# Kernel optimization log

Hardware: AMD Instinct MI355X
Metric: run time of the kernel (lower is better)

The kernel has to match this reference:

```python
import jax, jax.numpy as jnp
import numpy as np

B, S, K, D = 512, 64, 8, 16
NE, NR, NU = 2_000_000, 64, 10_000
NSTEPS, NUNITS, NITER = 100, 128, 2


def _alpha_schedule():
    # betas = sigmoid(linspace(-6,6)) * (0.005 - 1e-5) + 1e-5; alphas_prod = cumprod(1-betas)
    betas = jax.nn.sigmoid(jnp.linspace(-6.0, 6.0, NSTEPS)) * (0.005 - 1e-5) + 1e-5
    aprod = jnp.cumprod(1.0 - betas)
    return jnp.sqrt(aprod), jnp.sqrt(1.0 - aprod)


def _forward(usr_emb, ent_emb, rel_emb, agg_W, agg_b, fc1_W, fc1_b, fc2_W, fc2_b,
             mlp_W1, mlp_b1, mlp_W2, mlp_b2, mlp_W3, mlp_b3, mlp_W4, mlp_b4,
             step_emb1, step_emb2, step_emb3, noise_e, u, v, click_seq, adj_ent, adj_rel, t):
    user = usr_emb[u]                                   # [B,D]
    # --- diffusion branch: x = x0*sqrt(abar_t) + e*sqrt(1-abar_t), then MLP with step-emb adds
    abar_sqrt, ombar_sqrt = _alpha_schedule()
    x = user * abar_sqrt[t][:, None] + noise_e * ombar_sqrt[t][:, None]
    for Wl, bl, se in ((mlp_W1, mlp_b1, step_emb1), (mlp_W2, mlp_b2, step_emb2), (mlp_W3, mlp_b3, step_emb3)):
        x = jax.nn.relu(x @ Wl + bl + se[t])            # [B,128]
    diff_out = x @ mlp_W4 + mlp_b4                      # [B,D]
    # --- multi-hop neighbor gather (entities/relations per hop)
    e0 = click_seq                                      # [B,S]
    e1 = adj_ent[e0]                                    # [B,S,K]
    e2 = adj_ent[e1].reshape(B, S, K * K)               # [B,S,K*K]
    r0 = adj_rel[e0]                                    # [B,S,K]
    r1 = adj_rel[e1].reshape(B, S, K * K)               # [B,S,K*K]
    ev = [ent_emb[e0][:, :, None, :], ent_emb[e1], ent_emb[e2]]  # [B,S,1,D],[B,S,K,D],[B,S,K*K,D]
    rv = [rel_emb[r0], rel_emb[r1]]

    def aggregate(self_v, neigh_v, rel_v, act):
        # KGCN sum-aggregator: user-relation score softmax over neighbors, weighted sum, linear, act
        scores = jnp.mean(user[:, None, None, None, :] * rel_v, axis=-1)   # [B,S,n,K]
        p = jax.nn.softmax(scores, axis=-1)
        neigh_agg = jnp.einsum('bsnk,bsnkd->bsnd', p, neigh_v)             # [B,S,n,D]
        return act((self_v + neigh_agg) @ agg_W + agg_b)

    for i in range(NITER):
        act = jnp.tanh if i == NITER - 1 else jax.nn.sigmoid
        nxt = []
        for hop in range(NITER - i):
            n_self = ev[hop].shape[2]
            nv = ev[hop + 1].reshape(B, S, n_self, K, D)
            relv = rv[hop].reshape(B, S, n_self, K, D)
            nxt.append(aggregate(ev[hop], nv, relv, act))
        ev = nxt
    item_emb = jax.nn.relu(ev[0].reshape(B, S, D))      # relu applied twice in source == once
    trans = item_emb                                    # Transform treated as identity (code unavailable)
    s_sum = jax.nn.relu(jnp.sum(trans, axis=1))         # [B,D]
    s_max = jax.nn.relu(jnp.max(trans, axis=1))         # [B,D]
    fusion = jnp.concatenate([s_sum, s_max], axis=1)    # [B,2D]
    feat = jax.nn.relu(jax.nn.relu(fusion @ fc1_W + fc1_b) @ fc2_W + fc2_b)  # [B,D]
    outs = jax.nn.sigmoid(jnp.sum(feat * ent_emb[v], axis=1))               # [B]
    return jnp.concatenate([outs[:, None], diff_out], axis=1)               # [B,1+D]


def setup_inputs() -> dict:
    key = jax.random.key(0)
    ks = iter(jax.random.split(key, 32))
    nrm = lambda shape, s: jax.random.normal(next(ks), shape, dtype=jnp.float32) * s
    zf = lambda shape: jnp.zeros(shape, dtype=jnp.float32)
    ri = lambda shape, hi: jax.random.randint(next(ks), shape, 0, hi, dtype=jnp.int32)
    return {
        'usr_emb': nrm((NU, D), 0.1), 'ent_emb': nrm((NE, D), 0.1), 'rel_emb': nrm((NR, D), 0.1),
        'agg_W': nrm((D, D), 0.25), 'agg_b': zf((D,)),
        'fc1_W': nrm((2 * D, 64), 0.18), 'fc1_b': zf((64,)),
        'fc2_W': nrm((64, D), 0.125), 'fc2_b': zf((D,)),
        'mlp_W1': nrm((D, NUNITS), 0.25), 'mlp_b1': zf((NUNITS,)),
        'mlp_W2': nrm((NUNITS, NUNITS), 0.09), 'mlp_b2': zf((NUNITS,)),
        'mlp_W3': nrm((NUNITS, NUNITS), 0.09), 'mlp_b3': zf((NUNITS,)),
        'mlp_W4': nrm((NUNITS, D), 0.09), 'mlp_b4': zf((D,)),
        'step_emb1': nrm((NSTEPS, NUNITS), 0.1), 'step_emb2': nrm((NSTEPS, NUNITS), 0.1),
        'step_emb3': nrm((NSTEPS, NUNITS), 0.1),
        'noise_e': jax.random.normal(next(ks), (B, D), dtype=jnp.float32),
        'u': ri((B,), NU), 'v': ri((B,), NE), 'click_seq': ri((B, S), NE),
        'adj_ent': ri((NE, K), NE), 'adj_rel': ri((NE, K), NR), 't': ri((B,), NSTEPS),
    }


def reference(usr_emb, ent_emb, rel_emb, agg_W, agg_b, fc1_W, fc1_b, fc2_W, fc2_b,
              mlp_W1, mlp_b1, mlp_W2, mlp_b2, mlp_W3, mlp_b3, mlp_W4, mlp_b4,
              step_emb1, step_emb2, step_emb3, noise_e, u, v, click_seq, adj_ent, adj_rel, t):
    return _forward(usr_emb, ent_emb, rel_emb, agg_W, agg_b, fc1_W, fc1_b, fc2_W, fc2_b,
                    mlp_W1, mlp_b1, mlp_W2, mlp_b2, mlp_W3, mlp_b3, mlp_W4, mlp_b4,
                    step_emb1, step_emb2, step_emb3, noise_e, u, v, click_seq, adj_ent, adj_rel, t)
```

## Files before the change

### kernel.cpp

```cpp
#include <hip/hip_runtime.h>
#include <math.h>

namespace {
constexpr int B = 512, S = 64, K = 8, D = 16, NR = 64, NSTEPS = 100, NUNITS = 128;
}

#define WAVE_LDS_FENCE() __asm__ volatile("s_waitcnt lgkmcnt(0)" ::: "memory")

__global__ __launch_bounds__(256) void k_prep_all(
    const float* __restrict__ usr_emb, const float* __restrict__ rel_emb,
    const int* __restrict__ u, const int* __restrict__ click_seq,
    const int* __restrict__ adj_ent, const int* __restrict__ adj_rel,
    float* __restrict__ w_tab, int* __restrict__ e1s, int* __restrict__ r0s,
    float* __restrict__ sa, float* __restrict__ so)
{
    int b = blockIdx.x, t = threadIdx.x;
    if (t < 64) {
        const float* ur = usr_emb + (long)u[b] * D;
        const float* rr = rel_emb + t * D;
        float s = 0.f;
#pragma unroll
        for (int d = 0; d < D; ++d) s += ur[d] * rr[d];
        w_tab[b * NR + t] = s * (1.0f / 16.0f);
    } else if (t < 128) {
        int p = b * S + (t - 64);
        int e0 = click_seq[p];
        const int4* ae = (const int4*)(adj_ent + (long)e0 * K);
        const int4* ar = (const int4*)(adj_rel + (long)e0 * K);
        int4 a0 = ae[0], a1 = ae[1], b0 = ar[0], b1 = ar[1];
        int4* oe = (int4*)(e1s + (long)p * K);
        int4* orr = (int4*)(r0s + (long)p * K);
        oe[0] = a0; oe[1] = a1;
        orr[0] = b0; orr[1] = b1;
    } else if (b == 0 && (t - 128) < NSTEPS) {
        int i = t - 128;
        float prod = 1.0f;
        for (int jj = 0; jj <= i; ++jj) {
            float x = -6.0f + (float)jj * (12.0f / 99.0f);
            float sig = 1.0f / (1.0f + expf(-x));
            prod *= (1.0f - (sig * (0.005f - 1e-5f) + 1e-5f));
        }
        sa[i] = sqrtf(prod);
        so[i] = sqrtf(1.0f - prod);
    }
}

__global__ __launch_bounds__(256) void k_kgcn(
    const float* __restrict__ ent_emb,
    const float* __restrict__ w_tab,
    const int* __restrict__ click_seq,
    const int* __restrict__ adj_ent,
    const int* __restrict__ adj_rel,
    const int* __restrict__ e1s,
    const int* __restrict__ r0s,
    const float* __restrict__ agg_W,
    const float* __restrict__ agg_b,
    float* __restrict__ item)
{
    __shared__ float wb[4][NR];
    __shared__ float Ws[4][D][D + 1];
    __shared__ float bs[4][D];
    __shared__ float Ms[4][K][D + 1];
    __shared__ float h1s[4][K][D + 1];
    __shared__ float h0s[4][D];
    __shared__ float A0s[4][D];
    __shared__ float M1s[4][D];
    __shared__ float p0s[4][K];

    const int tid = threadIdx.x;
    const int w = tid >> 6;
    const int lane = tid & 63;
    const int p = blockIdx.x * 4 + w;
    const int b = p >> 6;
    const int k = lane >> 3, j = lane & 7;

    const int e0 = click_seq[p];
    const int e1k = e1s[(long)p * K + k];
    const int r0k = r0s[(long)p * K + k];
    const int e2kj = adj_ent[(long)e1k * K + j];
    const int r1kj = adj_rel[(long)e1k * K + j];

    {
        const float4 wv = ((const float4*)agg_W)[lane];
        int row = lane >> 2, col = (lane & 3) * 4;
        Ws[w][row][col] = wv.x; Ws[w][row][col + 1] = wv.y;
        Ws[w][row][col + 2] = wv.z; Ws[w][row][col + 3] = wv.w;
        wb[w][lane] = w_tab[b * NR + lane];
        if (lane < D) bs[w][lane] = agg_b[lane];
    }
    WAVE_LDS_FENCE();

    float s1 = wb[w][r1kj];
    float m1 = s1;
    m1 = fmaxf(m1, __shfl_xor(m1, 1));
    m1 = fmaxf(m1, __shfl_xor(m1, 2));
    m1 = fmaxf(m1, __shfl_xor(m1, 4));
    float ex = expf(s1 - m1);
    float den = ex;
    den += __shfl_xor(den, 1);
    den += __shfl_xor(den, 2);
    den += __shfl_xor(den, 4);
    float p1 = ex / den;

    float q2r[D], q1r[D], q0r[D];
    {
        const float4* q2p = (const float4*)(ent_emb + (long)e2kj * D);
        float4 a0 = q2p[0], a1 = q2p[1], a2 = q2p[2], a3 = q2p[3];
        q2r[0]=a0.x; q2r[1]=a0.y; q2r[2]=a0.z; q2r[3]=a0.w;
        q2r[4]=a1.x; q2r[5]=a1.y; q2r[6]=a1.z; q2r[7]=a1.w;
        q2r[8]=a2.x; q2r[9]=a2.y; q2r[10]=a2.z; q2r[11]=a2.w;
        q2r[12]=a3.x; q2r[13]=a3.y; q2r[14]=a3.z; q2r[15]=a3.w;
    }
    {
        const float4* q1p = (const float4*)(ent_emb + (long)e1k * D);
        float4 a0 = q1p[0], a1 = q1p[1], a2 = q1p[2], a3 = q1p[3];
        q1r[0]=a0.x; q1r[1]=a0.y; q1r[2]=a0.z; q1r[3]=a0.w;
        q1r[4]=a1.x; q1r[5]=a1.y; q1r[6]=a1.z; q1r[7]=a1.w;
        q1r[8]=a2.x; q1r[9]=a2.y; q1r[10]=a2.z; q1r[11]=a2.w;
        q1r[12]=a3.x; q1r[13]=a3.y; q1r[14]=a3.z; q1r[15]=a3.w;
    }
    {
        const float4* q0p = (const float4*)(ent_emb + (long)e0 * D);
        float4 a0 = q0p[0], a1 = q0p[1], a2 = q0p[2], a3 = q0p[3];
        q0r[0]=a0.x; q0r[1]=a0.y; q0r[2]=a0.z; q0r[3]=a0.w;
        q0r[4]=a1.x; q0r[5]=a1.y; q0r[6]=a1.z; q0r[7]=a1.w;
        q0r[8]=a2.x; q0r[9]=a2.y; q0r[10]=a2.z; q0r[11]=a2.w;
        q0r[12]=a3.x; q0r[13]=a3.y; q0r[14]=a3.z; q0r[15]=a3.w;
    }

    {
        float cur[16];
#pragma unroll
        for (int d = 0; d < 16; ++d) cur[d] = p1 * q2r[d];
        const bool b0 = (lane & 1), b1 = (lane & 2), b2 = (lane & 4);
        float n8[8];
#pragma unroll
        for (int d = 0; d < 8; ++d) {
            float snd = b0 ? cur[d] : cur[d + 8];
            float kp  = b0 ? cur[d + 8] : cur[d];
            n8[d] = kp + __shfl_xor(snd, 1);
        }
        float n4[4];
#pragma unroll
        for (int d = 0; d < 4; ++d) {
            float snd = b1 ? n8[d] : n8[d + 4];
            float kp  = b1 ? n8[d + 4] : n8[d];
            n4[d] = kp + __shfl_xor(snd, 2);
        }
        float a0 = (b2 ? n4[2] : n4[0]) + __shfl_xor(b2 ? n4[0] : n4[2], 4);
        float a1 = (b2 ? n4[3] : n4[1]) + __shfl_xor(b2 ? n4[1] : n4[3], 4);
        const int dbase = (b0 ? 8 : 0) + (b1 ? 4 : 0) + (b2 ? 2 : 0);
        Ms[w][k][dbase]     = q1r[dbase]     + a0;
        Ms[w][k][dbase + 1] = q1r[dbase + 1] + a1;
    }

    float s0 = wb[w][r0k];
    float m0 = s0;
    m0 = fmaxf(m0, __shfl_xor(m0, 8));
    m0 = fmaxf(m0, __shfl_xor(m0, 16));
    m0 = fmaxf(m0, __shfl_xor(m0, 32));
    float e0x = expf(s0 - m0);
    float d0 = e0x;
    d0 += __shfl_xor(d0, 8);
    d0 += __shfl_xor(d0, 16);
    d0 += __shfl_xor(d0, 32);
    float p0 = e0x / d0;
    if (j == 0) p0s[w][k] = p0;

    {
        float cur[16];
#pragma unroll
        for (int d = 0; d < 16; ++d) cur[d] = p0 * q1r[d];
        const bool c0 = (lane & 8), c1 = (lane & 16), c2 = (lane & 32);
        float n8[8];
#pragma unroll
        for (int d = 0; d < 8; ++d) {
            float snd = c0 ? cur[d] : cur[d + 8];
            float kp  = c0 ? cur[d + 8] : cur[d];
            n8[d] = kp + __shfl_xor(snd, 8);
        }
        float n4[4];
#pragma unroll
        for (int d = 0; d < 4; ++d) {
            float snd = c1 ? n8[d] : n8[d + 4];
            float kp  = c1 ? n8[d + 4] : n8[d];
            n4[d] = kp + __shfl_xor(snd, 16);
        }
        float a0 = (c2 ? n4[2] : n4[0]) + __shfl_xor(c2 ? n4[0] : n4[2], 32);
        float a1 = (c2 ? n4[3] : n4[1]) + __shfl_xor(c2 ? n4[1] : n4[3], 32);
        const int dbase = (c0 ? 8 : 0) + (c1 ? 4 : 0) + (c2 ? 2 : 0);
        if (j == 0) { A0s[w][dbase] = a0; A0s[w][dbase + 1] = a1; }
    }
    WAVE_LDS_FENCE();

#pragma unroll
    for (int o = lane; o < 128; o += 64) {
        int ko = o >> 4, dd = o & 15;
        float acc = bs[w][dd];
#pragma unroll
        for (int din = 0; din < D; ++din) acc += Ms[w][ko][din] * Ws[w][din][dd];
        h1s[w][ko][dd] = 1.0f / (1.0f + expf(-acc));
    }

    const int ddl = lane & 15;
    {
        float acc = bs[w][ddl];
#pragma unroll
        for (int din = 0; din < D; ++din)
            acc += (q0r[din] + A0s[w][din]) * Ws[w][din][ddl];
        if (lane < D) h0s[w][lane] = 1.0f / (1.0f + expf(-acc));
    }
    WAVE_LDS_FENCE();

    if (lane < D) {
        float m = h0s[w][lane];
#pragma unroll
        for (int kk = 0; kk < K; ++kk) m += p0s[w][kk] * h1s[w][kk][lane];
        M1s[w][lane] = m;
    }
    WAVE_LDS_FENCE();

    {
        float acc = bs[w][ddl];
#pragma unroll
        for (int din = 0; din < D; ++din) acc += M1s[w][din] * Ws[w][din][ddl];
        if (lane < D) item[(long)p * D + lane] = fmaxf(tanhf(acc), 0.0f);
    }
}

__global__ __launch_bounds__(128) void k_tail(
    const float* __restrict__ item,
    const float* __restrict__ fc1_W, const float* __restrict__ fc1_b,
    const float* __restrict__ fc2_W, const float* __restrict__ fc2_b,
    const float* __restrict__ ent_emb, const int* __restrict__ v,
    const float* __restrict__ usr_emb, const float* __restrict__ noise_e,
    const int* __restrict__ u, const int* __restrict__ t_arr,
    const float* __restrict__ W1, const float* __restrict__ b1,
    const float* __restrict__ W2, const float* __restrict__ b2,
    const float* __restrict__ W3, const float* __restrict__ b3,
    const float* __restrict__ W4, const float* __restrict__ b4,
    const float* __restrict__ se1, const float* __restrict__ se2,
    const float* __restrict__ se3,
    const float* __restrict__ sa, const float* __restrict__ so,
    float* __restrict__ out)
{
    __shared__ float x0[D];
    __shared__ float ha[NUNITS];
    __shared__ float hb[NUNITS];
    __shared__ float sm[S][D + 1];
    __shared__ float fus[2 * D];
    __shared__ float hid[64];
    __shared__ float feat_s[D];

    int b = blockIdx.x, t = threadIdx.x;
    int ts = t_arr[b];

    if (t < D)
        x0[t] = usr_emb[(long)u[b] * D + t] * sa[ts] + noise_e[(long)b * D + t] * so[ts];
    __syncthreads();

    float a = b1[t] + se1[(long)ts * NUNITS + t];
#pragma unroll
    for (int i = 0; i < D; ++i) a += x0[i] * W1[i * NUNITS + t];
    ha[t] = fmaxf(a, 0.0f);
    __syncthreads();

    a = b2[t] + se2[(long)ts * NUNITS + t];
    for (int i = 0; i < NUNITS; ++i) a += ha[i] * W2[i * NUNITS + t];
    hb[t] = fmaxf(a, 0.0f);
    __syncthreads();

    a = b3[t] + se3[(long)ts * NUNITS + t];
    for (int i = 0; i < NUNITS; ++i) a += hb[i] * W3[i * NUNITS + t];
    __syncthreads();
    ha[t] = fmaxf(a, 0.0f);
    __syncthreads();

    if (t < D) {
        float acc = b4[t];
        for (int i = 0; i < NUNITS; ++i) acc += ha[i] * W4[i * D + t];
        out[(long)b * 17 + 1 + t] = acc;
    }

    if (t < 64) {
        const float4* ip = (const float4*)(item + ((long)b * S + t) * D);
        float4 r0 = ip[0], r1 = ip[1], r2 = ip[2], r3 = ip[3];
        sm[t][0]=r0.x;  sm[t][1]=r0.y;  sm[t][2]=r0.z;  sm[t][3]=r0.w;
        sm[t][4]=r1.x;  sm[t][5]=r1.y;  sm[t][6]=r1.z;  sm[t][7]=r1.w;
        sm[t][8]=r2.x;  sm[t][9]=r2.y;  sm[t][10]=r2.z; sm[t][11]=r2.w;
        sm[t][12]=r3.x; sm[t][13]=r3.y; sm[t][14]=r3.z; sm[t][15]=r3.w;
    }
    __syncthreads();

    if (t < D) {
        float sv = 0.0f, mv = -1e30f;
        for (int ss = 0; ss < S; ++ss) {
            float x = sm[ss][t];
            sv += x;
            mv = fmaxf(mv, x);
        }
        fus[t] = fmaxf(sv, 0.0f);
        fus[D + t] = fmaxf(mv, 0.0f);
    }
    __syncthreads();

    if (t < 64) {
        float acc = fc1_b[t];
#pragma unroll
        for (int i = 0; i < 2 * D; ++i) acc += fus[i] * fc1_W[i * 64 + t];
        hid[t] = fmaxf(acc, 0.0f);
    }
    __syncthreads();

    if (t < D) {
        float f = fc2_b[t];
#pragma unroll
        for (int i = 0; i < 64; ++i) f += hid[i] * fc2_W[i * D + t];
        feat_s[t] = fmaxf(f, 0.0f);
    }
    __syncthreads();

    if (t < D) {
        float g = feat_s[t] * ent_emb[(long)v[b] * D + t];
        g += __shfl_xor(g, 1);
        g += __shfl_xor(g, 2);
        g += __shfl_xor(g, 4);
        g += __shfl_xor(g, 8);
        if (t == 0) out[(long)b * 17] = 1.0f / (1.0f + expf(-g));
    }
}

extern "C" void kernel_launch(void* const* d_in, const int* in_sizes, int n_in,
                              void* d_out, int out_size, void* d_ws, size_t ws_size,
                              hipStream_t stream) {
    const float* usr_emb = (const float*)d_in[0];
    const float* ent_emb = (const float*)d_in[1];
    const float* rel_emb = (const float*)d_in[2];
    const float* agg_W   = (const float*)d_in[3];
    const float* agg_b   = (const float*)d_in[4];
    const float* fc1_W   = (const float*)d_in[5];
    const float* fc1_b   = (const float*)d_in[6];
    const float* fc2_W   = (const float*)d_in[7];
    const float* fc2_b   = (const float*)d_in[8];
    const float* mlp_W1  = (const float*)d_in[9];
    const float* mlp_b1  = (const float*)d_in[10];
    const float* mlp_W2  = (const float*)d_in[11];
    const float* mlp_b2  = (const float*)d_in[12];
    const float* mlp_W3  = (const float*)d_in[13];
    const float* mlp_b3  = (const float*)d_in[14];
    const float* mlp_W4  = (const float*)d_in[15];
    const float* mlp_b4  = (const float*)d_in[16];
    const float* se1     = (const float*)d_in[17];
    const float* se2     = (const float*)d_in[18];
    const float* se3     = (const float*)d_in[19];
    const float* noise_e = (const float*)d_in[20];
    const int* u         = (const int*)d_in[21];
    const int* v         = (const int*)d_in[22];
    const int* click_seq = (const int*)d_in[23];
    const int* adj_ent   = (const int*)d_in[24];
    const int* adj_rel   = (const int*)d_in[25];
    const int* t         = (const int*)d_in[26];
    float* out = (float*)d_out;

    float* ws = (float*)d_ws;
    float* w_tab = ws;
    float* sa    = w_tab + B * NR;
    float* so    = sa + 128;
    float* item  = so + 128;
    int*   e1s   = (int*)(item + B * S * D);
    int*   r0s   = e1s + B * S * K;

    k_prep_all<<<B, 256, 0, stream>>>(usr_emb, rel_emb, u, click_seq, adj_ent, adj_rel,
                                      w_tab, e1s, r0s, sa, so);
    k_kgcn<<<(B * S) / 4, 256, 0, stream>>>(ent_emb, w_tab, click_seq, adj_ent, adj_rel,
                                            e1s, r0s, agg_W, agg_b, item);
    k_tail<<<B, 128, 0, stream>>>(item, fc1_W, fc1_b, fc2_W, fc2_b, ent_emb, v,
                                  usr_emb, noise_e, u, t, mlp_W1, mlp_b1, mlp_W2, mlp_b2,
                                  mlp_W3, mlp_b3, mlp_W4, mlp_b4, se1, se2, se3, sa, so, out);
}
```

Baseline: 337.4 us.

## Streamline KGCN aggregation LDS use and split tail MLP across 256 threads

The KGCN kernel now stores a transposed weight tile that each lane loads as a float4 column, and reads the relation-score row straight from global memory instead of staging it in LDS. Hop-1 outputs are combined with p0 through shuffles rather than LDS round trips, which removes two LDS fences and several shared arrays. The tail kernel doubles its block to 256 threads, splits the 128-wide matvecs into two halves reduced through shared memory, and runs the feature-pooling/fc branch alongside the diffusion MLP. This cuts per-block serial latency, at the cost of extra syncthreads and more register pressure from holding the weight column.

```diff
diff --git a/kernel.cpp b/kernel.cpp
--- a/kernel.cpp
+++ b/kernel.cpp
@@ -6,6 +6,16 @@
 }
 
 #define WAVE_LDS_FENCE() __asm__ volatile("s_waitcnt lgkmcnt(0)" ::: "memory")
+
+#define LOAD16(dst, ptr)                                                     \
+    {                                                                        \
+        const float4* _p = (const float4*)(ptr);                             \
+        float4 _a = _p[0], _b = _p[1], _c = _p[2], _d = _p[3];               \
+        dst[0] = _a.x;  dst[1] = _a.y;  dst[2] = _a.z;  dst[3] = _a.w;       \
+        dst[4] = _b.x;  dst[5] = _b.y;  dst[6] = _b.z;  dst[7] = _b.w;       \
+        dst[8] = _c.x;  dst[9] = _c.y;  dst[10] = _c.z; dst[11] = _c.w;      \
+        dst[12] = _d.x; dst[13] = _d.y; dst[14] = _d.z; dst[15] = _d.w;      \
+    }
 
 __global__ __launch_bounds__(256) void k_prep_all(
     const float* __restrict__ usr_emb, const float* __restrict__ rel_emb,
@@ -57,15 +67,11 @@
     const float* __restrict__ agg_b,
     float* __restrict__ item)
 {
-    __shared__ float wb[4][NR];
-    __shared__ float Ws[4][D][D + 1];
+    __shared__ __attribute__((aligned(16))) float Wt[4][D][20];
+    __shared__ __attribute__((aligned(16))) float Ms[4][K][20];
+    __shared__ __attribute__((aligned(16))) float A0s[4][D];
+    __shared__ __attribute__((aligned(16))) float M1s[4][D];
     __shared__ float bs[4][D];
-    __shared__ float Ms[4][K][D + 1];
-    __shared__ float h1s[4][K][D + 1];
-    __shared__ float h0s[4][D];
-    __shared__ float A0s[4][D];
-    __shared__ float M1s[4][D];
-    __shared__ float p0s[4][K];
 
     const int tid = threadIdx.x;
     const int w = tid >> 6;
@@ -83,50 +89,32 @@
     {
         const float4 wv = ((const float4*)agg_W)[lane];
         int row = lane >> 2, col = (lane & 3) * 4;
-        Ws[w][row][col] = wv.x; Ws[w][row][col + 1] = wv.y;
-        Ws[w][row][col + 2] = wv.z; Ws[w][row][col + 3] = wv.w;
-        wb[w][lane] = w_tab[b * NR + lane];
+        Wt[w][col][row]     = wv.x;
+        Wt[w][col + 1][row] = wv.y;
+        Wt[w][col + 2][row] = wv.z;
+        Wt[w][col + 3][row] = wv.w;
         if (lane < D) bs[w][lane] = agg_b[lane];
     }
-    WAVE_LDS_FENCE();
-
-    float s1 = wb[w][r1kj];
-    float m1 = s1;
-    m1 = fmaxf(m1, __shfl_xor(m1, 1));
-    m1 = fmaxf(m1, __shfl_xor(m1, 2));
-    m1 = fmaxf(m1, __shfl_xor(m1, 4));
-    float ex = expf(s1 - m1);
+
+    const float* wrow = w_tab + (long)b * NR;
+    const float s1 = wrow[r1kj];
+    const float s0 = wrow[r0k];
+
+    float m1x = s1;
+    m1x = fmaxf(m1x, __shfl_xor(m1x, 1));
+    m1x = fmaxf(m1x, __shfl_xor(m1x, 2));
+    m1x = fmaxf(m1x, __shfl_xor(m1x, 4));
+    float ex = expf(s1 - m1x);
     float den = ex;
     den += __shfl_xor(den, 1);
     den += __shfl_xor(den, 2);
     den += __shfl_xor(den, 4);
     float p1 = ex / den;
 
-    float q2r[D], q1r[D], q0r[D];
-    {
-        const float4* q2p = (const float4*)(ent_emb + (long)e2kj * D);
-        float4 a0 = q2p[0], a1 = q2p[1], a2 = q2p[2], a3 = q2p[3];
-        q2r[0]=a0.x; q2r[1]=a0.y; q2r[2]=a0.z; q2r[3]=a0.w;
-        q2r[4]=a1.x; q2r[5]=a1.y; q2r[6]=a1.z; q2r[7]=a1.w;
-        q2r[8]=a2.x; q2r[9]=a2.y; q2r[10]=a2.z; q2r[11]=a2.w;
-        q2r[12]=a3.x; q2r[13]=a3.y; q2r[14]=a3.z; q2r[15]=a3.w;
-    }
-    {
-        const float4* q1p = (const float4*)(ent_emb + (long)e1k * D);
-        float4 a0 = q1p[0], a1 = q1p[1], a2 = q1p[2], a3 = q1p[3];
-        q1r[0]=a0.x; q1r[1]=a0.y; q1r[2]=a0.z; q1r[3]=a0.w;
-        q1r[4]=a1.x; q1r[5]=a1.y; q1r[6]=a1.z; q1r[7]=a1.w;
-        q1r[8]=a2.x; q1r[9]=a2.y; q1r[10]=a2.z; q1r[11]=a2.w;
-        q1r[12]=a3.x; q1r[13]=a3.y; q1r[14]=a3.z; q1r[15]=a3.w;
-    }
-    {
-        const float4* q0p = (const float4*)(ent_emb + (long)e0 * D);
-        float4 a0 = q0p[0], a1 = q0p[1], a2 = q0p[2], a3 = q0p[3];
-        q0r[0]=a0.x; q0r[1]=a0.y; q0r[2]=a0.z; q0r[3]=a0.w;
-        q0r[4]=a1.x; q0r[5]=a1.y; q0r[6]=a1.z; q0r[7]=a1.w;
-        q0r[8]=a2.x; q0r[9]=a2.y; q0r[10]=a2.z; q0r[11]=a2.w;
-        q0r[12]=a3.x; q0r[13]=a3.y; q0r[14]=a3.z; q0r[15]=a3.w;
-    }
+    float q2r[16], q1r[16], q0r[16];
+    LOAD16(q2r, ent_emb + (long)e2kj * D);
+    LOAD16(q1r, ent_emb + (long)e1k * D);
+    LOAD16(q0r, ent_emb + (long)e0 * D);
 
     {
         float cur[16];
@@ -150,11 +138,9 @@
         float a0 = (b2 ? n4[2] : n4[0]) + __shfl_xor(b2 ? n4[0] : n4[2], 4);
         float a1 = (b2 ? n4[3] : n4[1]) + __shfl_xor(b2 ? n4[1] : n4[3], 4);
         const int dbase = (b0 ? 8 : 0) + (b1 ? 4 : 0) + (b2 ? 2 : 0);
-        Ms[w][k][dbase]     = q1r[dbase]     + a0;
-        Ms[w][k][dbase + 1] = q1r[dbase + 1] + a1;
-    }
-
-    float s0 = wb[w][r0k];
+        *(float2*)&Ms[w][k][dbase] = make_float2(q1r[dbase] + a0, q1r[dbase + 1] + a1);
+    }
+
     float m0 = s0;
     m0 = fmaxf(m0, __shfl_xor(m0, 8));
     m0 = fmaxf(m0, __shfl_xor(m0, 16));
@@ -165,7 +151,6 @@
     d0 += __shfl_xor(d0, 16);
     d0 += __shfl_xor(d0, 32);
     float p0 = e0x / d0;
-    if (j == 0) p0s[w][k] = p0;
 
     {
         float cur[16];
@@ -189,46 +174,65 @@
         float a0 = (c2 ? n4[2] : n4[0]) + __shfl_xor(c2 ? n4[0] : n4[2], 32);
         float a1 = (c2 ? n4[3] : n4[1]) + __shfl_xor(c2 ? n4[1] : n4[3], 32);
         const int dbase = (c0 ? 8 : 0) + (c1 ? 4 : 0) + (c2 ? 2 : 0);
-        if (j == 0) { A0s[w][dbase] = a0; A0s[w][dbase + 1] = a1; }
+        if (j == 0) *(float2*)&A0s[w][dbase] = make_float2(a0, a1);
     }
     WAVE_LDS_FENCE();
 
-#pragma unroll
-    for (int o = lane; o < 128; o += 64) {
-        int ko = o >> 4, dd = o & 15;
-        float acc = bs[w][dd];
-#pragma unroll
-        for (int din = 0; din < D; ++din) acc += Ms[w][ko][din] * Ws[w][din][dd];
-        h1s[w][ko][dd] = 1.0f / (1.0f + expf(-acc));
-    }
-
     const int ddl = lane & 15;
-    {
-        float acc = bs[w][ddl];
-#pragma unroll
-        for (int din = 0; din < D; ++din)
-            acc += (q0r[din] + A0s[w][din]) * Ws[w][din][ddl];
-        if (lane < D) h0s[w][lane] = 1.0f / (1.0f + expf(-acc));
-    }
+    const int g = lane >> 4;
+
+    float wc[16];
+    LOAD16(wc, &Wt[w][ddl][0]);
+    const float bias = bs[w][ddl];
+
+    float h1a, h1b;
+    {
+        float mr[16];
+        LOAD16(mr, &Ms[w][g][0]);
+        float acc = bias;
+#pragma unroll
+        for (int i = 0; i < 16; ++i) acc += mr[i] * wc[i];
+        h1a = 1.0f / (1.0f + expf(-acc));
+    }
+    {
+        float mr[16];
+        LOAD16(mr, &Ms[w][g + 4][0]);
+        float acc = bias;
+#pragma unroll
+        for (int i = 0; i < 16; ++i) acc += mr[i] * wc[i];
+        h1b = 1.0f / (1.0f + expf(-acc));
+    }
+
+    float h0v;
+    {
+        float ar[16];
+        LOAD16(ar, &A0s[w][0]);
+        float acc = bias;
+#pragma unroll
+        for (int i = 0; i < 16; ++i) acc += (q0r[i] + ar[i]) * wc[i];
+        h0v = 1.0f / (1.0f + expf(-acc));
+    }
+
+    const float p0a = __shfl(p0, g * 8);
+    const float p0b = __shfl(p0, g * 8 + 32);
+    float part = p0a * h1a + p0b * h1b;
+    part += __shfl_xor(part, 16);
+    part += __shfl_xor(part, 32);
+    const float m1v = h0v + part;
+    if (lane < D) M1s[w][lane] = m1v;
     WAVE_LDS_FENCE();
 
-    if (lane < D) {
-        float m = h0s[w][lane];
-#pragma unroll
-        for (int kk = 0; kk < K; ++kk) m += p0s[w][kk] * h1s[w][kk][lane];
-        M1s[w][lane] = m;
-    }
-    WAVE_LDS_FENCE();
-
-    {
-        float acc = bs[w][ddl];
-#pragma unroll
-        for (int din = 0; din < D; ++din) acc += M1s[w][din] * Ws[w][din][ddl];
+    {
+        float mr[16];
+        LOAD16(mr, &M1s[w][0]);
+        float acc = bias;
+#pragma unroll
+        for (int i = 0; i < 16; ++i) acc += mr[i] * wc[i];
         if (lane < D) item[(long)p * D + lane] = fmaxf(tanhf(acc), 0.0f);
     }
 }
 
-__global__ __launch_bounds__(128) void k_tail(
+__global__ __launch_bounds__(256) void k_tail(
     const float* __restrict__ item,
     const float* __restrict__ fc1_W, const float* __restrict__ fc1_b,
     const float* __restrict__ fc2_W, const float* __restrict__ fc2_b,
@@ -245,89 +249,107 @@
     float* __restrict__ out)
 {
     __shared__ float x0[D];
-    __shared__ float ha[NUNITS];
-    __shared__ float hb[NUNITS];
+    __shared__ float v1[NUNITS], v2[NUNITS], v3[NUNITS];
+    __shared__ float pp[2][NUNITS];
     __shared__ float sm[S][D + 1];
     __shared__ float fus[2 * D];
     __shared__ float hid[64];
     __shared__ float feat_s[D];
 
-    int b = blockIdx.x, t = threadIdx.x;
-    int ts = t_arr[b];
-
-    if (t < D)
-        x0[t] = usr_emb[(long)u[b] * D + t] * sa[ts] + noise_e[(long)b * D + t] * so[ts];
-    __syncthreads();
-
-    float a = b1[t] + se1[(long)ts * NUNITS + t];
-#pragma unroll
-    for (int i = 0; i < D; ++i) a += x0[i] * W1[i * NUNITS + t];
-    ha[t] = fmaxf(a, 0.0f);
-    __syncthreads();
-
-    a = b2[t] + se2[(long)ts * NUNITS + t];
-    for (int i = 0; i < NUNITS; ++i) a += ha[i] * W2[i * NUNITS + t];
-    hb[t] = fmaxf(a, 0.0f);
-    __syncthreads();
-
-    a = b3[t] + se3[(long)ts * NUNITS + t];
-    for (int i = 0; i < NUNITS; ++i) a += hb[i] * W3[i * NUNITS + t];
-    __syncthreads();
-    ha[t] = fmaxf(a, 0.0f);
-    __syncthreads();
-
-    if (t < D) {
-        float acc = b4[t];
-        for (int i = 0; i < NUNITS; ++i) acc += ha[i] * W4[i * D + t];
-        out[(long)b * 17 + 1 + t] = acc;
-    }
-
-    if (t < 64) {
-        const float4* ip = (const float4*)(item + ((long)b * S + t) * D);
+    const int b = blockIdx.x, tid = threadIdx.x;
+    const int t = tid & 127, h = tid >> 7;
+    const int ts = t_arr[b];
+
+    if (tid < D)
+        x0[tid] = usr_emb[(long)u[b] * D + tid] * sa[ts] + noise_e[(long)b * D + tid] * so[ts];
+    if (tid >= 128 && tid < 192) {
+        int ss = tid - 128;
+        const float4* ip = (const float4*)(item + ((long)b * S + ss) * D);
         float4 r0 = ip[0], r1 = ip[1], r2 = ip[2], r3 = ip[3];
-        sm[t][0]=r0.x;  sm[t][1]=r0.y;  sm[t][2]=r0.z;  sm[t][3]=r0.w;
-        sm[t][4]=r1.x;  sm[t][5]=r1.y;  sm[t][6]=r1.z;  sm[t][7]=r1.w;
-        sm[t][8]=r2.x;  sm[t][9]=r2.y;  sm[t][10]=r2.z; sm[t][11]=r2.w;
-        sm[t][12]=r3.x; sm[t][13]=r3.y; sm[t][14]=r3.z; sm[t][15]=r3.w;
-    }
-    __syncthreads();
-
-    if (t < D) {
+        sm[ss][0]=r0.x;  sm[ss][1]=r0.y;  sm[ss][2]=r0.z;  sm[ss][3]=r0.w;
+        sm[ss][4]=r1.x;  sm[ss][5]=r1.y;  sm[ss][6]=r1.z;  sm[ss][7]=r1.w;
+        sm[ss][8]=r2.x;  sm[ss][9]=r2.y;  sm[ss][10]=r2.z; sm[ss][11]=r2.w;
+        sm[ss][12]=r3.x; sm[ss][13]=r3.y; sm[ss][14]=r3.z; sm[ss][15]=r3.w;
+    }
+    __syncthreads();
+
+    if (h == 0) {
+        float a = b1[t] + se1[(long)ts * NUNITS + t];
+#pragma unroll
+        for (int i = 0; i < D; ++i) a += x0[i] * W1[i * NUNITS + t];
+        v1[t] = fmaxf(a, 0.0f);
+    } else if (tid >= 192 && tid < 192 + D) {
+        int d = tid - 192;
         float sv = 0.0f, mv = -1e30f;
+#pragma unroll
         for (int ss = 0; ss < S; ++ss) {
-            float x = sm[ss][t];
+            float x = sm[ss][d];
             sv += x;
             mv = fmaxf(mv, x);
         }
-        fus[t] = fmaxf(sv, 0.0f);
-        fus[D + t] = fmaxf(mv, 0.0f);
-    }
-    __syncthreads();
-
-    if (t < 64) {
-        float acc = fc1_b[t];
-#pragma unroll
-        for (int i = 0; i < 2 * D; ++i) acc += fus[i] * fc1_W[i * 64 + t];
-        hid[t] = fmaxf(acc, 0.0f);
-    }
-    __syncthreads();
-
-    if (t < D) {
-        float f = fc2_b[t];
-#pragma unroll
-        for (int i = 0; i < 64; ++i) f += hid[i] * fc2_W[i * D + t];
-        feat_s[t] = fmaxf(f, 0.0f);
-    }
-    __syncthreads();
-
-    if (t < D) {
-        float g = feat_s[t] * ent_emb[(long)v[b] * D + t];
-        g += __shfl_xor(g, 1);
-        g += __shfl_xor(g, 2);
-        g += __shfl_xor(g, 4);
-        g += __shfl_xor(g, 8);
-        if (t == 0) out[(long)b * 17] = 1.0f / (1.0f + expf(-g));
-    }
+        fus[d] = fmaxf(sv, 0.0f);
+        fus[D + d] = fmaxf(mv, 0.0f);
+    }
+    __syncthreads();
+
+    {
+        float part = 0.0f;
+        const float* wp = W2 + (long)(64 * h) * NUNITS + t;
+#pragma unroll 8
+        for (int i = 0; i < 64; ++i) part += v1[64 * h + i] * wp[(long)i * NUNITS];
+        pp[h][t] = part;
+    }
+    __syncthreads();
+
+    if (tid < NUNITS) {
+        v2[tid] = fmaxf(b2[tid] + se2[(long)ts * NUNITS + tid] + pp[0][tid] + pp[1][tid], 0.0f);
+    } else if (tid < 192) {
+        int o = tid - 128;
+        float acc = fc1_b[o];
+#pragma unroll
+        for (int i = 0; i < 2 * D; ++i) acc += fus[i] * fc1_W[i * 64 + o];
+        hid[o] = fmaxf(acc, 0.0f);
+    }
+    __syncthreads();
+
+    {
+        float part = 0.0f;
+        const float* wp = W3 + (long)(64 * h) * NUNITS + t;
+#pragma unroll 8
+        for (int i = 0; i < 64; ++i) part += v2[64 * h + i] * wp[(long)i * NUNITS];
+        pp[h][t] = part;
+    }
+    __syncthreads();
+
+    if (tid < NUNITS) {
+        v3[tid] = fmaxf(b3[tid] + se3[(long)ts * NUNITS + tid] + pp[0][tid] + pp[1][tid], 0.0f);
+    } else if (tid >= 192 && tid < 192 + D) {
+        int d = tid - 192;
+        float f = fc2_b[d];
+#pragma unroll
+        for (int i = 0; i < 64; ++i) f += hid[i] * fc2_W[i * D + d];
+        feat_s[d] = fmaxf(f, 0.0f);
+    }
+    __syncthreads();
+
+    if (tid < 32) {
+        int o = tid & 15, hh = tid >> 4;
+        float acc = 0.0f;
+#pragma unroll
+        for (int i = 0; i < 64; ++i) acc += v3[64 * hh + i] * W4[(64 * hh + i) * D + o];
+        pp[hh][o] = acc;
+    } else if (tid >= 192 && tid < 192 + D) {
+        int d = tid - 192;
+        float gv = feat_s[d] * ent_emb[(long)v[b] * D + d];
+        gv += __shfl_xor(gv, 1);
+        gv += __shfl_xor(gv, 2);
+        gv += __shfl_xor(gv, 4);
+        gv += __shfl_xor(gv, 8);
+        if (d == 0) out[(long)b * 17] = 1.0f / (1.0f + expf(-gv));
+    }
+    __syncthreads();
+
+    if (tid < D) out[(long)b * 17 + 1 + tid] = b4[tid] + pp[0][tid] + pp[1][tid];
 }
 
 extern "C" void kernel_launch(void* const* d_in, const int* in_sizes, int n_in,
@@ -374,7 +396,7 @@
                                       w_tab, e1s, r0s, sa, so);
     k_kgcn<<<(B * S) / 4, 256, 0, stream>>>(ent_emb, w_tab, click_seq, adj_ent, adj_rel,
                                             e1s, r0s, agg_W, agg_b, item);
-    k_tail<<<B, 128, 0, stream>>>(item, fc1_W, fc1_b, fc2_W, fc2_b, ent_emb, v,
+    k_tail<<<B, 256, 0, stream>>>(item, fc1_W, fc1_b, fc2_W, fc2_b, ent_emb, v,
                                   usr_emb, noise_e, u, t, mlp_W1, mlp_b1, mlp_W2, mlp_b2,
                                   mlp_W3, mlp_b3, mlp_W4, mlp_b4, se1, se2, se3, sa, so, out);
 }
```

Result: no change. 344.1 us (+2.0%).
